# Optimization experiments

Measured on AMD Instinct MI355X. Metric: run time of the kernel, lower is better.

Reference implementation:

```python
import jax, jax.numpy as jnp
import numpy as np

B, N, NC = 16, 102000, 35        # batch, raw YOLOv7@1280 predictions, num classes
IMG = 1280                        # input image size
CONF_THRESH = 0.25
IOU_THRESH = 0.45
PRE_TOPK = 1024                   # candidates kept before IoU suppression (yolov7 max_nms analogue)
MAX_DET = 300                     # padded detections per image (yolov7 max_det)


def setup_inputs() -> dict:
    key = jax.random.key(0)
    kxy, kwh, kobj, kcls = jax.random.split(key, 4)
    xy = jax.random.uniform(kxy, (B, N, 2), dtype=jnp.float32) * IMG        # box centers in pixels
    wh = jax.random.uniform(kwh, (B, N, 2), dtype=jnp.float32) * 96.0 + 4.0  # box sizes
    obj = jax.random.uniform(kobj, (B, N, 1), dtype=jnp.float32)            # objectness
    cls = jax.random.uniform(kcls, (B, N, NC), dtype=jnp.float32)           # class scores
    pred = jnp.concatenate([xy, wh, obj, cls], axis=-1)  # [B, N, 5+NC]
    return {"pred": pred}


def _xywh2xyxy(xywh):
    xy, wh = xywh[..., :2], xywh[..., 2:4]
    return jnp.concatenate([xy - wh * 0.5, xy + wh * 0.5], axis=-1)


def _iou_matrix(b):
    # b: [K, 4] xyxy -> [K, K] pairwise IoU
    area = jnp.clip(b[:, 2] - b[:, 0], 0.0) * jnp.clip(b[:, 3] - b[:, 1], 0.0)
    lt = jnp.maximum(b[:, None, :2], b[None, :, :2])
    rb = jnp.minimum(b[:, None, 2:], b[None, :, 2:])
    wh = jnp.clip(rb - lt, 0.0)
    inter = wh[..., 0] * wh[..., 1]
    return inter / (area[:, None] + area[None, :] - inter + 1e-7)


def _nms_single(boxes, scores, cls_id):
    # boxes: [N,4] xyxy, scores: [N] (0 where below conf thresh), cls_id: [N] float
    s, idx = jax.lax.top_k(scores, PRE_TOPK)
    b = boxes[idx]
    c = cls_id[idx]
    iou = _iou_matrix(b)              # [K, K]
    valid = s > 0.0
    ar = jnp.arange(PRE_TOPK)

    def body(suppressed, i):
        keep_i = valid[i] & ~suppressed[i]
        suppressed = suppressed | (keep_i & (iou[i] > IOU_THRESH) & (ar > i))
        return suppressed, keep_i

    _, keep = jax.lax.scan(body, jnp.zeros(PRE_TOPK, bool), ar)
    final = jnp.where(keep, s, 0.0)
    fs, fidx = jax.lax.top_k(final, MAX_DET)
    # [MAX_DET, 6] = x1, y1, x2, y2, conf, cls (conf==0 rows are padding)
    return jnp.concatenate([b[fidx], fs[:, None], c[fidx][:, None]], axis=-1)


def reference(pred):
    # yolov7 non_max_suppression, class-agnostic, best-class per box
    boxes = _xywh2xyxy(pred[..., :4])                    # [B, N, 4]
    obj = pred[..., 4]                                   # [B, N]
    cls_scores = pred[..., 5:] * obj[..., None]          # obj_conf * cls_conf
    conf = jnp.max(cls_scores, axis=-1)                  # [B, N]
    cls_id = jnp.argmax(cls_scores, axis=-1).astype(pred.dtype)
    cand = (obj > CONF_THRESH) & (conf > CONF_THRESH)    # candidate filter
    scores = jnp.where(cand, conf, 0.0)
    return jax.vmap(_nms_single)(boxes, scores, cls_id)  # [B, MAX_DET, 6]
```

## Files before the change

kernel.cpp:

```cpp
#include <hip/hip_runtime.h>
#include <stdint.h>

#define BB 16
#define NN 102000
#define NCLS 35
#define RSTRIDE 40
#define PRE 1024
#define CAP 2048
#define MAXDET 300
#define NBUCK 4096
#define CONF_T 0.25f
#define IOU_T 0.45f
#define BUCK_BASE 0x3E800000u
#define SROWS 256

#define SCORES_OFF ((size_t)0)
#define SCORES_BYTES ((size_t)BB * NN * 4)
#define GHIST_OFF (SCORES_OFF + SCORES_BYTES)
#define GHIST_BYTES ((size_t)BB * NBUCK * 4)
#define CUT_OFF (GHIST_OFF + GHIST_BYTES)
#define BOXES_OFF (CUT_OFF + 64)
#define BOXES_BYTES ((size_t)BB * PRE * 16)
#define SVAL_OFF (BOXES_OFF + BOXES_BYTES)
#define SVAL_BYTES ((size_t)BB * PRE * 4)
#define CLS_OFF (SVAL_OFF + SVAL_BYTES)
#define CLS_BYTES ((size_t)BB * PRE * 4)
#define MASK_OFF (CLS_OFF + CLS_BYTES)
#define MASK_BYTES ((size_t)BB * PRE * 16 * 8)

__global__ __launch_bounds__(256) void k_score(const float* __restrict__ pred,
                                               float* __restrict__ scores,
                                               unsigned int* __restrict__ ghist) {
    __shared__ float4 lds4[SROWS * 9];
    int b = blockIdx.y, tid = threadIdx.x;
    int rowBase = blockIdx.x * SROWS;
    int nrows = NN - rowBase; if (nrows > SROWS) nrows = SROWS;
    const float4* gp = (const float4*)(pred + ((size_t)b * NN + rowBase) * RSTRIDE);
    int nf4 = nrows * 9;
    for (int it = tid; it < nf4; it += 256) {
        int r = it / 9;
        int c = it - r * 9;
        lds4[r * 9 + c] = gp[r * 10 + 1 + c];
    }
    __syncthreads();
    if (tid < nrows) {
        const float4* row4 = &lds4[tid * 9];
        float4 v0 = row4[0];
        float obj = v0.x;
        float score = 0.0f;
        if (obj > CONF_T) {
            float best = v0.y * obj;
            best = fmaxf(best, v0.z * obj);
            best = fmaxf(best, v0.w * obj);
#pragma unroll
            for (int c = 1; c < 9; ++c) {
                float4 v = row4[c];
                best = fmaxf(best, v.x * obj);
                best = fmaxf(best, v.y * obj);
                best = fmaxf(best, v.z * obj);
                best = fmaxf(best, v.w * obj);
            }
            if (best > CONF_T) score = best;
        }
        scores[(size_t)b * NN + rowBase + tid] = score;
        if (score > 0.0f) {
            unsigned int bits = __float_as_uint(score);
            unsigned int bk = (bits - BUCK_BASE) >> 12;
            if (bk > NBUCK - 1u) bk = NBUCK - 1u;
            atomicAdd(&ghist[b * NBUCK + bk], 1u);
        }
    }
}

__global__ __launch_bounds__(1024) void k_cut(const unsigned int* __restrict__ ghist,
                                              unsigned int* __restrict__ cutv) {
    __shared__ int sA[1024], sB[1024];
    __shared__ int cutB;
    int b = blockIdx.x, tid = threadIdx.x;
    if (tid == 0) cutB = 0;
    __syncthreads();
    const unsigned int* gh = ghist + b * NBUCK;
    int h0 = gh[4 * tid + 0], h1 = gh[4 * tid + 1];
    int h2 = gh[4 * tid + 2], h3 = gh[4 * tid + 3];
    sA[tid] = h0 + h1 + h2 + h3;
    __syncthreads();
    int* src = sA;
    int* dst = sB;
    for (int off = 1; off < 1024; off <<= 1) {
        int x = src[tid];
        if (tid + off < 1024) x += src[tid + off];
        dst[tid] = x;
        __syncthreads();
        int* t_ = src; src = dst; dst = t_;
    }
    int nxt = (tid + 1 < 1024) ? src[tid + 1] : 0;
    int s3 = h3 + nxt;
    int s2 = h2 + s3;
    int s1 = h1 + s2;
    int s0 = h0 + s1;
    if (s0 >= PRE && s1 < PRE) cutB = 4 * tid + 0;
    if (s1 >= PRE && s2 < PRE) cutB = 4 * tid + 1;
    if (s2 >= PRE && s3 < PRE) cutB = 4 * tid + 2;
    if (s3 >= PRE && nxt < PRE) cutB = 4 * tid + 3;
    __syncthreads();
    if (tid == 0) cutv[b] = (unsigned int)cutB;
}

__global__ __launch_bounds__(1024) void k_sort(const float* __restrict__ scores,
                                               const unsigned int* __restrict__ cutv,
                                               const float* __restrict__ pred,
                                               float4* __restrict__ boxesWS,
                                               float* __restrict__ svalWS,
                                               float* __restrict__ clsWS) {
    __shared__ unsigned long long keys[CAP];
    __shared__ unsigned int nloc;
    int b = blockIdx.x, tid = threadIdx.x;
    unsigned int cut = cutv[b];
    if (tid == 0) nloc = 0u;
    for (int k = tid; k < CAP; k += 1024) keys[k] = 0ull;
    __syncthreads();
    const float4* sb4 = (const float4*)(scores + (size_t)b * NN);
    for (int it = tid; it < NN / 4; it += 1024) {
        float4 s4 = sb4[it];
        float sv[4] = {s4.x, s4.y, s4.z, s4.w};
#pragma unroll
        for (int u = 0; u < 4; ++u) {
            float s = sv[u];
            if (s > 0.0f) {
                unsigned int bits = __float_as_uint(s);
                unsigned int bk = (bits - BUCK_BASE) >> 12;
                if (bk > NBUCK - 1u) bk = NBUCK - 1u;
                if (bk >= cut) {
                    unsigned int pos = atomicAdd(&nloc, 1u);
                    unsigned int idx = (unsigned int)(it * 4 + u);
                    if (pos < CAP)
                        keys[pos] = ((unsigned long long)bits << 32) |
                                    (unsigned int)(~idx);
                }
            }
        }
    }
    __syncthreads();
    for (int k = 2; k <= CAP; k <<= 1) {
        for (int j = k >> 1; j > 0; j >>= 1) {
            int p = ((tid & ~(j - 1)) << 1) | (tid & (j - 1));
            int q = p | j;
            unsigned long long a = keys[p], c = keys[q];
            bool desc = (p & k) == 0;
            bool sw = desc ? (a < c) : (a > c);
            if (sw) { keys[p] = c; keys[q] = a; }
            __syncthreads();
        }
    }
    unsigned long long key = keys[tid];
    unsigned int bits = (unsigned int)(key >> 32);
    unsigned int idx = ~(unsigned int)key;
    float sc = __uint_as_float(bits);
    if (bits == 0u || idx >= NN) { idx = 0; sc = 0.0f; }
    const float4* row = (const float4*)(pred + ((size_t)b * NN + idx) * RSTRIDE);
    float4 r0 = row[0];
    float4 r1 = row[1];
    float obj = r1.x;
    float best = r1.y * obj; int bj = 0;
    float p1 = r1.z * obj; if (p1 > best) { best = p1; bj = 1; }
    float p2 = r1.w * obj; if (p2 > best) { best = p2; bj = 2; }
#pragma unroll
    for (int kk = 2; kk <= 9; ++kk) {
        float4 r = row[kk];
        int base = (kk - 2) * 4 + 3;
        float q0 = r.x * obj; if (q0 > best) { best = q0; bj = base + 0; }
        float q1 = r.y * obj; if (q1 > best) { best = q1; bj = base + 1; }
        float q2 = r.z * obj; if (q2 > best) { best = q2; bj = base + 2; }
        float q3 = r.w * obj; if (q3 > best) { best = q3; bj = base + 3; }
    }
    float hx = r0.z * 0.5f;
    float hy = r0.w * 0.5f;
    boxesWS[b * PRE + tid] = make_float4(r0.x - hx, r0.y - hy, r0.x + hx, r0.y + hy);
    svalWS[b * PRE + tid] = sc;
    clsWS[b * PRE + tid] = (float)bj;
}

__global__ __launch_bounds__(256) void k_mask(const float4* __restrict__ boxesWS,
                                              const float* __restrict__ svalWS,
                                              unsigned long long* __restrict__ maskC) {
    __shared__ float bx1[PRE], by1[PRE], bx2[PRE], by2[PRE], bar[PRE], bsv[PRE];
    int b = blockIdx.y, tid = threadIdx.x;
    for (int i = tid; i < PRE; i += 256) {
        float4 bx = boxesWS[b * PRE + i];
        bx1[i] = bx.x; by1[i] = bx.y; bx2[i] = bx.z; by2[i] = bx.w;
        float aw = fmaxf(bx.z - bx.x, 0.0f);
        float ah = fmaxf(bx.w - bx.y, 0.0f);
        bar[i] = aw * ah;
        bsv[i] = svalWS[b * PRE + i];
    }
    __syncthreads();
    int j = blockIdx.x * 4 + (tid >> 6);
    int lane = tid & 63;
    float jx1 = bx1[j], jy1 = by1[j], jx2 = bx2[j], jy2 = by2[j], ja = bar[j];
    unsigned long long* out = maskC + ((size_t)b * PRE + j) * 16;
    for (int c = 0; c < 16; ++c) {
        unsigned long long word = 0ull;
        if (c * 64 < j) {
            int i = c * 64 + lane;
            bool bit = false;
            if (i < j && bsv[i] > 0.0f) {
                float ltx = fmaxf(bx1[i], jx1), lty = fmaxf(by1[i], jy1);
                float rbx = fminf(bx2[i], jx2), rby = fminf(by2[i], jy2);
                float wx = fmaxf(rbx - ltx, 0.0f);
                float wy = fmaxf(rby - lty, 0.0f);
                float inter = wx * wy;
                float denom = ((bar[i] + ja) - inter) + 1e-7f;
                bit = (inter / denom) > IOU_T;
            }
            word = __ballot(bit);
        }
        if (lane == 0) out[c] = word;
    }
}

__global__ __launch_bounds__(1024) void k_nms_out(const float4* __restrict__ boxesWS,
                                                  const float* __restrict__ svalWS,
                                                  const float* __restrict__ clsWS,
                                                  const unsigned long long* __restrict__ maskC,
                                                  float* __restrict__ out) {
    __shared__ unsigned long long supp[16], nsupp[16];
    __shared__ int changed;
    __shared__ int wtot[16], woff[17];
    int b = blockIdx.x, tid = threadIdx.x;
    int lane = tid & 63, w = tid >> 6;
    unsigned long long cm[16];
    const unsigned long long* mrow = maskC + ((size_t)b * PRE + tid) * 16;
#pragma unroll
    for (int k = 0; k < 16; ++k) cm[k] = mrow[k];
    float sv = svalWS[b * PRE + tid];
    if (tid < 16) supp[tid] = 0ull;
    __syncthreads();
    for (int it = 0; it < PRE + 2; ++it) {
        bool nb = false;
#pragma unroll
        for (int k = 0; k < 16; ++k) nb |= ((cm[k] & ~supp[k]) != 0ull);
        unsigned long long word = __ballot(nb);
        __syncthreads();
        if (lane == 0) nsupp[w] = word;
        if (tid == 0) changed = 0;
        __syncthreads();
        if (tid < 16) {
            if (nsupp[tid] != supp[tid]) changed = 1;
            supp[tid] = nsupp[tid];
        }
        __syncthreads();
        if (!changed) break;
    }
    bool keep = (sv > 0.0f) && !((supp[w] >> lane) & 1ull);
    unsigned long long km = __ballot(keep);
    int lp = __popcll(km & ((lane == 0) ? 0ull : ((1ull << lane) - 1ull)));
    if (lane == 0) wtot[w] = __popcll(km);
    __syncthreads();
    if (tid == 0) {
        int acc = 0;
        for (int k = 0; k < 16; ++k) { woff[k] = acc; acc += wtot[k]; }
        woff[16] = acc;
    }
    __syncthreads();
    int K = woff[16];
    int keptExcl = woff[w] + lp;
    int slot = keep ? keptExcl : (K + (tid - keptExcl));
    if (slot < MAXDET) {
        float4 bx = boxesWS[b * PRE + tid];
        float cv = clsWS[b * PRE + tid];
        float* o = out + ((size_t)b * MAXDET + slot) * 6;
        o[0] = bx.x; o[1] = bx.y; o[2] = bx.z; o[3] = bx.w;
        o[4] = keep ? sv : 0.0f;
        o[5] = cv;
    }
}

extern "C" void kernel_launch(void* const* d_in, const int* in_sizes, int n_in,
                              void* d_out, int out_size, void* d_ws, size_t ws_size,
                              hipStream_t stream) {
    const float* pred = (const float*)d_in[0];
    float* out = (float*)d_out;
    char* ws = (char*)d_ws;
    float* scores = (float*)(ws + SCORES_OFF);
    unsigned int* ghist = (unsigned int*)(ws + GHIST_OFF);
    unsigned int* cutv = (unsigned int*)(ws + CUT_OFF);
    float4* boxesWS = (float4*)(ws + BOXES_OFF);
    float* svalWS = (float*)(ws + SVAL_OFF);
    float* clsWS = (float*)(ws + CLS_OFF);
    unsigned long long* maskC = (unsigned long long*)(ws + MASK_OFF);

    hipMemsetAsync(ws + GHIST_OFF, 0, GHIST_BYTES, stream);
    k_score<<<dim3((NN + SROWS - 1) / SROWS, BB), 256, 0, stream>>>(pred, scores, ghist);
    k_cut<<<BB, 1024, 0, stream>>>(ghist, cutv);
    k_sort<<<BB, 1024, 0, stream>>>(scores, cutv, pred, boxesWS, svalWS, clsWS);
    k_mask<<<dim3(PRE / 4, BB), 256, 0, stream>>>(boxesWS, svalWS, maskC);
    k_nms_out<<<BB, 1024, 0, stream>>>(boxesWS, svalWS, clsWS, maskC, out);
}
```

Before: 436.5 us.

## Compact high-score candidates in scoring pass and fuse cut into sort kernel

The scoring kernel now appends candidates whose score bucket is above a fixed high threshold to a per-image global list, using a wave-aggregated atomic. The sort kernel can then gather from that short list instead of rescanning all 102k scores. The cut computation is merged into the sort kernel, removing one launch. Bitonic sort keys get padded shared-memory indexing to reduce bank conflicts, and the NMS fixpoint loop drops one barrier per iteration. A fallback full scan is kept for when the cut is below the threshold or the list overflows.

After: 631.0 us. +44.6%, slower.

```diff
diff --git a/kernel.cpp b/kernel.cpp
--- a/kernel.cpp
+++ b/kernel.cpp
@@ -13,13 +13,16 @@
 #define IOU_T 0.45f
 #define BUCK_BASE 0x3E800000u
 #define SROWS 256
+#define HI_BUCK 3584u
+#define GL_CAP 16384
 
 #define SCORES_OFF ((size_t)0)
 #define SCORES_BYTES ((size_t)BB * NN * 4)
 #define GHIST_OFF (SCORES_OFF + SCORES_BYTES)
 #define GHIST_BYTES ((size_t)BB * NBUCK * 4)
-#define CUT_OFF (GHIST_OFF + GHIST_BYTES)
-#define BOXES_OFF (CUT_OFF + 64)
+#define GCNT_OFF (GHIST_OFF + GHIST_BYTES)
+#define GCNT_BYTES ((size_t)64)
+#define BOXES_OFF (GCNT_OFF + GCNT_BYTES)
 #define BOXES_BYTES ((size_t)BB * PRE * 16)
 #define SVAL_OFF (BOXES_OFF + BOXES_BYTES)
 #define SVAL_BYTES ((size_t)BB * PRE * 4)
@@ -27,10 +30,17 @@
 #define CLS_BYTES ((size_t)BB * PRE * 4)
 #define MASK_OFF (CLS_OFF + CLS_BYTES)
 #define MASK_BYTES ((size_t)BB * PRE * 16 * 8)
+#define GLIST_OFF (MASK_OFF + MASK_BYTES)
+#define GLIST_BYTES ((size_t)BB * GL_CAP * 8)
+
+__device__ __forceinline__ int KS(int i) { return i + (i >> 4); }
+#define CAPP (CAP + (CAP >> 4))
 
 __global__ __launch_bounds__(256) void k_score(const float* __restrict__ pred,
                                                float* __restrict__ scores,
-                                               unsigned int* __restrict__ ghist) {
+                                               unsigned int* __restrict__ ghist,
+                                               unsigned int* __restrict__ gcnt,
+                                               unsigned long long* __restrict__ glist) {
     __shared__ float4 lds4[SROWS * 9];
     int b = blockIdx.y, tid = threadIdx.x;
     int rowBase = blockIdx.x * SROWS;
@@ -43,11 +53,12 @@
         lds4[r * 9 + c] = gp[r * 10 + 1 + c];
     }
     __syncthreads();
+    float score = 0.0f;
+    unsigned int bits = 0u, bk = 0u;
     if (tid < nrows) {
         const float4* row4 = &lds4[tid * 9];
         float4 v0 = row4[0];
         float obj = v0.x;
-        float score = 0.0f;
         if (obj > CONF_T) {
             float best = v0.y * obj;
             best = fmaxf(best, v0.z * obj);
@@ -64,25 +75,50 @@
         }
         scores[(size_t)b * NN + rowBase + tid] = score;
         if (score > 0.0f) {
-            unsigned int bits = __float_as_uint(score);
-            unsigned int bk = (bits - BUCK_BASE) >> 12;
+            bits = __float_as_uint(score);
+            bk = (bits - BUCK_BASE) >> 12;
             if (bk > NBUCK - 1u) bk = NBUCK - 1u;
             atomicAdd(&ghist[b * NBUCK + bk], 1u);
         }
     }
-}
-
-__global__ __launch_bounds__(1024) void k_cut(const unsigned int* __restrict__ ghist,
-                                              unsigned int* __restrict__ cutv) {
+    bool want = (score > 0.0f) && (bk >= HI_BUCK);
+    unsigned long long m = __ballot(want);
+    int lane = tid & 63;
+    if (m != 0ull) {
+        int leader = __ffsll((long long)m) - 1;
+        unsigned int base = 0u;
+        if (lane == leader) base = atomicAdd(&gcnt[b], (unsigned int)__popcll(m));
+        base = __shfl(base, leader);
+        if (want) {
+            unsigned int pos = base + (unsigned int)__popcll(m & ((1ull << lane) - 1ull));
+            if (pos < GL_CAP)
+                glist[(size_t)b * GL_CAP + pos] =
+                    ((unsigned long long)bits << 32) |
+                    (unsigned int)(~(unsigned int)(rowBase + tid));
+        }
+    }
+}
+
+__global__ __launch_bounds__(1024) void k_sort(const float* __restrict__ scores,
+                                               const unsigned int* __restrict__ ghist,
+                                               const unsigned int* __restrict__ gcnt,
+                                               const unsigned long long* __restrict__ glist,
+                                               const float* __restrict__ pred,
+                                               float4* __restrict__ boxesWS,
+                                               float* __restrict__ svalWS,
+                                               float* __restrict__ clsWS) {
     __shared__ int sA[1024], sB[1024];
-    __shared__ int cutB;
+    __shared__ int cutSh;
+    __shared__ unsigned long long keys[CAPP];
+    __shared__ unsigned int nloc;
     int b = blockIdx.x, tid = threadIdx.x;
-    if (tid == 0) cutB = 0;
-    __syncthreads();
+
     const unsigned int* gh = ghist + b * NBUCK;
     int h0 = gh[4 * tid + 0], h1 = gh[4 * tid + 1];
     int h2 = gh[4 * tid + 2], h3 = gh[4 * tid + 3];
+    if (tid == 0) { cutSh = 0; nloc = 0u; }
     sA[tid] = h0 + h1 + h2 + h3;
+    for (int k = tid; k < CAP; k += 1024) keys[KS(k)] = 0ull;
     __syncthreads();
     int* src = sA;
     int* dst = sB;
@@ -98,61 +134,66 @@
     int s2 = h2 + s3;
     int s1 = h1 + s2;
     int s0 = h0 + s1;
-    if (s0 >= PRE && s1 < PRE) cutB = 4 * tid + 0;
-    if (s1 >= PRE && s2 < PRE) cutB = 4 * tid + 1;
-    if (s2 >= PRE && s3 < PRE) cutB = 4 * tid + 2;
-    if (s3 >= PRE && nxt < PRE) cutB = 4 * tid + 3;
-    __syncthreads();
-    if (tid == 0) cutv[b] = (unsigned int)cutB;
-}
-
-__global__ __launch_bounds__(1024) void k_sort(const float* __restrict__ scores,
-                                               const unsigned int* __restrict__ cutv,
-                                               const float* __restrict__ pred,
-                                               float4* __restrict__ boxesWS,
-                                               float* __restrict__ svalWS,
-                                               float* __restrict__ clsWS) {
-    __shared__ unsigned long long keys[CAP];
-    __shared__ unsigned int nloc;
-    int b = blockIdx.x, tid = threadIdx.x;
-    unsigned int cut = cutv[b];
-    if (tid == 0) nloc = 0u;
-    for (int k = tid; k < CAP; k += 1024) keys[k] = 0ull;
-    __syncthreads();
-    const float4* sb4 = (const float4*)(scores + (size_t)b * NN);
-    for (int it = tid; it < NN / 4; it += 1024) {
-        float4 s4 = sb4[it];
-        float sv[4] = {s4.x, s4.y, s4.z, s4.w};
-#pragma unroll
-        for (int u = 0; u < 4; ++u) {
-            float s = sv[u];
-            if (s > 0.0f) {
-                unsigned int bits = __float_as_uint(s);
-                unsigned int bk = (bits - BUCK_BASE) >> 12;
-                if (bk > NBUCK - 1u) bk = NBUCK - 1u;
-                if (bk >= cut) {
-                    unsigned int pos = atomicAdd(&nloc, 1u);
-                    unsigned int idx = (unsigned int)(it * 4 + u);
-                    if (pos < CAP)
-                        keys[pos] = ((unsigned long long)bits << 32) |
-                                    (unsigned int)(~idx);
+    if (s0 >= PRE && s1 < PRE) cutSh = 4 * tid + 0;
+    if (s1 >= PRE && s2 < PRE) cutSh = 4 * tid + 1;
+    if (s2 >= PRE && s3 < PRE) cutSh = 4 * tid + 2;
+    if (s3 >= PRE && nxt < PRE) cutSh = 4 * tid + 3;
+    __syncthreads();
+    unsigned int cut = (unsigned int)cutSh;
+    unsigned int gn = gcnt[b];
+
+    if (cut >= HI_BUCK && gn <= (unsigned int)GL_CAP) {
+        int n = (int)gn;
+        const unsigned long long* gl = glist + (size_t)b * GL_CAP;
+        for (int it = tid; it < n; it += 1024) {
+            unsigned long long key = gl[it];
+            unsigned int bits = (unsigned int)(key >> 32);
+            unsigned int bk = (bits - BUCK_BASE) >> 12;
+            if (bk > NBUCK - 1u) bk = NBUCK - 1u;
+            if (bk >= cut) {
+                unsigned int pos = atomicAdd(&nloc, 1u);
+                if (pos < CAP) keys[KS((int)pos)] = key;
+            }
+        }
+    } else {
+        const float4* sb4 = (const float4*)(scores + (size_t)b * NN);
+        for (int it = tid; it < NN / 4; it += 1024) {
+            float4 s4 = sb4[it];
+            float sv[4] = {s4.x, s4.y, s4.z, s4.w};
+#pragma unroll
+            for (int u = 0; u < 4; ++u) {
+                float s = sv[u];
+                if (s > 0.0f) {
+                    unsigned int bits = __float_as_uint(s);
+                    unsigned int bk = (bits - BUCK_BASE) >> 12;
+                    if (bk > NBUCK - 1u) bk = NBUCK - 1u;
+                    if (bk >= cut) {
+                        unsigned int pos = atomicAdd(&nloc, 1u);
+                        unsigned int idx = (unsigned int)(it * 4 + u);
+                        if (pos < CAP)
+                            keys[KS((int)pos)] = ((unsigned long long)bits << 32) |
+                                                 (unsigned int)(~idx);
+                    }
                 }
             }
         }
     }
     __syncthreads();
+
     for (int k = 2; k <= CAP; k <<= 1) {
         for (int j = k >> 1; j > 0; j >>= 1) {
             int p = ((tid & ~(j - 1)) << 1) | (tid & (j - 1));
             int q = p | j;
-            unsigned long long a = keys[p], c = keys[q];
+            int pp = KS(p), qq = KS(q);
+            unsigned long long a = keys[pp], c = keys[qq];
             bool desc = (p & k) == 0;
             bool sw = desc ? (a < c) : (a > c);
-            if (sw) { keys[p] = c; keys[q] = a; }
+            if (sw) { keys[pp] = c; keys[qq] = a; }
             __syncthreads();
         }
     }
-    unsigned long long key = keys[tid];
+
+    unsigned long long key = keys[KS(tid)];
     unsigned int bits = (unsigned int)(key >> 32);
     unsigned int idx = ~(unsigned int)key;
     float sc = __uint_as_float(bits);
@@ -223,8 +264,8 @@
                                                   const float* __restrict__ clsWS,
                                                   const unsigned long long* __restrict__ maskC,
                                                   float* __restrict__ out) {
-    __shared__ unsigned long long supp[16], nsupp[16];
-    __shared__ int changed;
+    __shared__ unsigned long long supp[16];
+    __shared__ int lastch;
     __shared__ int wtot[16], woff[17];
     int b = blockIdx.x, tid = threadIdx.x;
     int lane = tid & 63, w = tid >> 6;
@@ -234,6 +275,7 @@
     for (int k = 0; k < 16; ++k) cm[k] = mrow[k];
     float sv = svalWS[b * PRE + tid];
     if (tid < 16) supp[tid] = 0ull;
+    if (tid == 0) lastch = -1;
     __syncthreads();
     for (int it = 0; it < PRE + 2; ++it) {
         bool nb = false;
@@ -241,15 +283,12 @@
         for (int k = 0; k < 16; ++k) nb |= ((cm[k] & ~supp[k]) != 0ull);
         unsigned long long word = __ballot(nb);
         __syncthreads();
-        if (lane == 0) nsupp[w] = word;
-        if (tid == 0) changed = 0;
+        if (lane == 0) {
+            if (word != supp[w]) lastch = it;
+            supp[w] = word;
+        }
         __syncthreads();
-        if (tid < 16) {
-            if (nsupp[tid] != supp[tid]) changed = 1;
-            supp[tid] = nsupp[tid];
-        }
-        __syncthreads();
-        if (!changed) break;
+        if (lastch != it) break;
     }
     bool keep = (sv > 0.0f) && !((supp[w] >> lane) & 1ull);
     unsigned long long km = __ballot(keep);
@@ -283,16 +322,18 @@
     char* ws = (char*)d_ws;
     float* scores = (float*)(ws + SCORES_OFF);
     unsigned int* ghist = (unsigned int*)(ws + GHIST_OFF);
-    unsigned int* cutv = (unsigned int*)(ws + CUT_OFF);
+    unsigned int* gcnt = (unsigned int*)(ws + GCNT_OFF);
     float4* boxesWS = (float4*)(ws + BOXES_OFF);
     float* svalWS = (float*)(ws + SVAL_OFF);
     float* clsWS = (float*)(ws + CLS_OFF);
     unsigned long long* maskC = (unsigned long long*)(ws + MASK_OFF);
-
-    hipMemsetAsync(ws + GHIST_OFF, 0, GHIST_BYTES, stream);
-    k_score<<<dim3((NN + SROWS - 1) / SROWS, BB), 256, 0, stream>>>(pred, scores, ghist);
-    k_cut<<<BB, 1024, 0, stream>>>(ghist, cutv);
-    k_sort<<<BB, 1024, 0, stream>>>(scores, cutv, pred, boxesWS, svalWS, clsWS);
+    unsigned long long* glist = (unsigned long long*)(ws + GLIST_OFF);
+
+    hipMemsetAsync(ws + GHIST_OFF, 0, GHIST_BYTES + GCNT_BYTES, stream);
+    k_score<<<dim3((NN + SROWS - 1) / SROWS, BB), 256, 0, stream>>>(pred, scores, ghist,
+                                                                   gcnt, glist);
+    k_sort<<<BB, 1024, 0, stream>>>(scores, ghist, gcnt, glist, pred,
+                                    boxesWS, svalWS, clsWS);
     k_mask<<<dim3(PRE / 4, BB), 256, 0, stream>>>(boxesWS, svalWS, maskC);
     k_nms_out<<<BB, 1024, 0, stream>>>(boxesWS, svalWS, clsWS, maskC, out);
 }
```
